# Performance work log

Measured on AMD Instinct MI355X. Metric: run time of the kernel, lower is better.

Reference implementation:

```python
import jax, jax.numpy as jnp
import numpy as np
from jax import lax

STRIDE = 2  # down_sample_stride
MATMUL_NORM = True


def maxpool2d_5d(x, s):
    # x: [B, T, C, H, W]; kernel=s, stride=s, padding=(s-1)//2 == 0 for s=2
    return lax.reduce_window(
        x, -jnp.inf, lax.max,
        window_dimensions=(1, 1, 1, s, s),
        window_strides=(1, 1, 1, s, s),
        padding='VALID')


def setup_inputs() -> dict:
    key = jax.random.key(0)
    k1, k2, k3, k4 = jax.random.split(key, 4)
    B, T, Ck, Cv, H, W = 2, 4, 64, 256, 64, 64
    return {
        'memory_keys': jax.random.normal(k1, (B, T, Ck, H, W), jnp.float32),
        'memory_values': jax.random.normal(k2, (B, T, Cv, H, W), jnp.float32),
        'query_key': jax.random.normal(k3, (B, Ck, H, W), jnp.float32),
        'query_value': jax.random.normal(k4, (B, Cv, H, W), jnp.float32),
    }


def reference(memory_keys, memory_values, query_key, query_value):
    B, T, Ck, oH, oW = memory_keys.shape
    Cv = memory_values.shape[2]
    # down-sample memory bank (max pool, stride 2, no padding)
    mk = maxpool2d_5d(memory_keys, STRIDE)   # [B,T,Ck,h,w]
    mv = maxpool2d_5d(memory_values, STRIDE) # [B,T,Cv,h,w]
    h, w = mk.shape[-2], mk.shape[-1]
    M = T * h * w
    N = oH * oH  # code uses ori_height*ori_height (square assumed)
    # permute(0,2,1,3,4).view(B,Ck,M).permute(0,2,1) -> [B, M, Ck]
    mk = mk.transpose(0, 2, 1, 3, 4).reshape(B, Ck, M).transpose(0, 2, 1)
    qk = query_key.reshape(B, Ck, N)
    attn = jnp.einsum('bmc,bcn->bmn', mk, qk)  # [B, M, N]
    if MATMUL_NORM:
        attn = attn * (Ck ** -0.5)
    attn = jax.nn.softmax(attn, axis=1)  # softmax over memory positions
    mv = mv.transpose(0, 2, 1, 3, 4).reshape(B, Cv, M)
    memory = jnp.einsum('bcm,bmn->bcn', mv, attn).reshape(B, Cv, oH, oW)
    return jnp.concatenate([query_value, memory], axis=1)  # [B, 2*Cv, H, W]
```

## Files before the change

### kernel.cpp

```cpp
#include <hip/hip_runtime.h>
#include <hip/hip_bf16.h>

typedef unsigned short u16;
typedef unsigned int   u32;
typedef __attribute__((ext_vector_type(8))) short  bf16x8;
typedef __attribute__((ext_vector_type(4))) float  floatx4;

#define NB 2
#define NT 4
#define CK 64
#define CV 256
#define HH 64
#define WW 64
#define MM 4096
#define NN 4096
#define SCALE 0.125f
#define SHIFT 4.0f
#define OUT_B 2097152
#define NW 32
#define NIT 32

__device__ __forceinline__ u16 f2b(float f) {
    __hip_bfloat16 h = __float2bfloat16(f);
    union { __hip_bfloat16 h; u16 u; } v; v.h = h; return v.u;
}

#define PRE_K 65536
#define PRE_V 589824
#define PRE_T 1114112

__global__ void prep(const float* __restrict__ mk, const float* __restrict__ mv,
                     const float4* __restrict__ qv,
                     u16* __restrict__ pk2, u16* __restrict__ vt,
                     float* __restrict__ out) {
    int u = blockIdx.x * 256 + threadIdx.x;
    if (u < PRE_K) {
        int m = u & 4095, cb8 = (u >> 12) & 7, b = u >> 15;
        int t = m >> 10, hh = (m >> 5) & 31, ww = m & 31;
        const float* s0 = mk + ((size_t)((b*NT + t)*CK + cb8*8))*(HH*WW)
                             + (2*hh)*WW + 2*ww;
        bf16x8 fr;
        #pragma unroll
        for (int i = 0; i < 8; ++i) {
            const float* s = s0 + (size_t)i*(HH*WW);
            float2 r0 = *(const float2*)s;
            float2 r1 = *(const float2*)(s + WW);
            fr[i] = (short)f2b(fmaxf(fmaxf(r0.x, r0.y), fmaxf(r1.x, r1.y)));
        }
        *(bf16x8*)(pk2 + ((size_t)(b*8 + cb8)*MM + m)*8) = fr;
    } else if (u < PRE_V) {
        int u2 = u - PRE_K;
        int m4 = u2 & 1023, c = (u2 >> 10) & 255, b = u2 >> 18;
        int t = m4 >> 8, hh = (m4 >> 3) & 31, w8 = m4 & 7;
        const float* s0 = mv + ((size_t)((b*NT + t)*CV + c))*(HH*WW)
                             + (2*hh)*WW + 8*w8;
        float4 a0 = *(const float4*)(s0);
        float4 a1 = *(const float4*)(s0 + 4);
        float4 b0 = *(const float4*)(s0 + WW);
        float4 b1 = *(const float4*)(s0 + WW + 4);
        ushort4 r;
        r.x = f2b(fmaxf(fmaxf(a0.x, a0.y), fmaxf(b0.x, b0.y)));
        r.y = f2b(fmaxf(fmaxf(a0.z, a0.w), fmaxf(b0.z, b0.w)));
        r.z = f2b(fmaxf(fmaxf(a1.x, a1.y), fmaxf(b1.x, b1.y)));
        r.w = f2b(fmaxf(fmaxf(a1.z, a1.w), fmaxf(b1.z, b1.w)));
        *(ushort4*)(vt + ((size_t)(b*CV + c)*MM) + m4*4) = r;
    } else {
        int u3 = u - PRE_V;
        int b = u3 >> 18, ru = u3 & 262143;
        ((float4*)out)[(size_t)b*(OUT_B/4) + ru] = qv[u3];
    }
}

__device__ __forceinline__ void qk_phase(bf16x8 k0, bf16x8 k1,
        const bf16x8 (&qf)[2][2], float (&sacc)[2],
        u16* __restrict__ Pd, int lrow, int cbw, int sw)
{
    #pragma unroll
    for (int t = 0; t < 2; ++t) {
        floatx4 s = __builtin_amdgcn_mfma_f32_16x16x32_bf16(
                        k0, qf[0][t], (floatx4){0.f,0.f,0.f,0.f}, 0, 0, 0);
        s = __builtin_amdgcn_mfma_f32_16x16x32_bf16(k1, qf[1][t], s, 0, 0, 0);
        float p0 = __expf(s[0]*SCALE - SHIFT);
        float p1 = __expf(s[1]*SCALE - SHIFT);
        float p2 = __expf(s[2]*SCALE - SHIFT);
        float p3 = __expf(s[3]*SCALE - SHIFT);
        sacc[t] += (p0 + p1) + (p2 + p3);
        u32 d0 = (u32)f2b(p0) | ((u32)f2b(p1) << 16);
        u32 d1 = (u32)f2b(p2) | ((u32)f2b(p3) << 16);
        *(uint2*)&Pd[(t*16 + lrow)*128 + ((cbw ^ sw) << 2)] = make_uint2(d0, d1);
    }
}

__device__ __forceinline__ void pv_phase(const bf16x8 (&vf)[4][2],
        floatx4 (&oacc)[2][2], const u16* __restrict__ Ps,
        int lrow, int quad, int sw)
{
    #pragma unroll
    for (int cc = 0; cc < 4; ++cc) {
        bf16x8 pf[2];
        #pragma unroll
        for (int t = 0; t < 2; ++t) {
            int cb = (cc << 3) + (quad << 1);
            pf[t] = *(const bf16x8*)&Ps[(t*16 + lrow)*128 + ((cb ^ sw) << 2)];
        }
        __builtin_amdgcn_s_setprio(1);
        #pragma unroll
        for (int j = 0; j < 2; ++j)
            #pragma unroll
            for (int t = 0; t < 2; ++t)
                oacc[j][t] = __builtin_amdgcn_mfma_f32_16x16x32_bf16(
                                 vf[cc][j], pf[t], oacc[j][t], 0, 0, 0);
        __builtin_amdgcn_s_setprio(0);
    }
}

__launch_bounds__(512, 2)
__global__ void attn_v2(const u16* __restrict__ pk2, const u16* __restrict__ vt,
                        const float* __restrict__ qk, float* __restrict__ out) {
    const int bid = blockIdx.x;
    const int xcd = bid & 7;
    const int b   = xcd >> 2;
    const int ntile = ((bid >> 3) << 2) + (xcd & 3);
    const int tid = threadIdx.x, w = tid >> 6, l = tid & 63;
    const int lrow = l & 15, quad = l >> 4;
    const int n0 = ntile * NW;
    const int sw = lrow << 1;
    const int cbw = (w << 2) + quad;

    __shared__ u16  P[2][NW * 128];
    __shared__ float sums_s[8][NW];

    bf16x8 qf[2][2];
    const float* qb = qk + (size_t)b * CK * NN + n0;
    #pragma unroll
    for (int cc = 0; cc < 2; ++cc)
        #pragma unroll
        for (int t = 0; t < 2; ++t)
            #pragma unroll
            for (int i = 0; i < 8; ++i) {
                int c = cc*32 + quad*8 + i;
                qf[cc][t][i] = (short)f2b(qb[(size_t)c*NN + t*16 + lrow]);
            }

    const u16* pkb  = pk2 + (size_t)b * (8*MM*8);
    const u16* vtb  = vt  + (size_t)b * CV * MM;
    const int  mrw  = w*16 + lrow;
    const u16* vrow = vtb + (size_t)(w*32 + lrow)*MM + quad*8;

    floatx4 oacc[2][2];
    #pragma unroll
    for (int j = 0; j < 2; ++j)
        #pragma unroll
        for (int t = 0; t < 2; ++t)
            oacc[j][t] = (floatx4){0.f, 0.f, 0.f, 0.f};
    float sacc[2] = {0.f, 0.f};

    bf16x8 vf[4][2];
    {
        bf16x8 k0 = *(const bf16x8*)(pkb + ((size_t)quad*MM + mrw)*8);
        bf16x8 k1 = *(const bf16x8*)(pkb + ((size_t)(quad+4)*MM + mrw)*8);
        #pragma unroll
        for (int cc = 0; cc < 4; ++cc)
            #pragma unroll
            for (int j = 0; j < 2; ++j)
                vf[cc][j] = *(const bf16x8*)(vrow + (size_t)j*(16*MM) + cc*32);
        qk_phase(k0, k1, qf, sacc, P[0], lrow, cbw, sw);
    }

    #pragma unroll 2
    for (int it = 0; it < NIT; ++it) {
        __syncthreads();
        const bool more = (it + 1 < NIT);
        bf16x8 k0n, k1n, vfn[4][2];
        if (more) {
            const int mb2 = (it + 1) << 7;
            k0n = *(const bf16x8*)(pkb + ((size_t)quad*MM + mb2 + mrw)*8);
            k1n = *(const bf16x8*)(pkb + ((size_t)(quad+4)*MM + mb2 + mrw)*8);
            #pragma unroll
            for (int cc = 0; cc < 4; ++cc)
                #pragma unroll
                for (int j = 0; j < 2; ++j)
                    vfn[cc][j] = *(const bf16x8*)(vrow + (size_t)j*(16*MM) + mb2 + cc*32);
        }
        pv_phase(vf, oacc, P[it & 1], lrow, quad, sw);
        if (more) {
            qk_phase(k0n, k1n, qf, sacc, P[(it + 1) & 1], lrow, cbw, sw);
            #pragma unroll
            for (int cc = 0; cc < 4; ++cc)
                #pragma unroll
                for (int j = 0; j < 2; ++j)
                    vf[cc][j] = vfn[cc][j];
        }
    }

    #pragma unroll
    for (int t = 0; t < 2; ++t) {
        float v = sacc[t];
        v += __shfl_xor(v, 16, 64);
        v += __shfl_xor(v, 32, 64);
        if (l < 16) sums_s[w][t*16 + l] = v;
    }
    __syncthreads();
    float inv[2];
    #pragma unroll
    for (int t = 0; t < 2; ++t) {
        float d = 0.f;
        #pragma unroll
        for (int w2 = 0; w2 < 8; ++w2) d += sums_s[w2][t*16 + lrow];
        inv[t] = 1.0f / d;
    }

    float* ob = out + ((size_t)(b*512 + 256))*NN + n0;
    #pragma unroll
    for (int j = 0; j < 2; ++j)
        #pragma unroll
        for (int t = 0; t < 2; ++t)
            #pragma unroll
            for (int r = 0; r < 4; ++r) {
                int c = w*32 + j*16 + quad*4 + r;
                ob[(size_t)c*NN + t*16 + lrow] = oacc[j][t][r] * inv[t];
            }
}


__global__ void pool_v_f32(const float* __restrict__ src, float* __restrict__ out) {
    int e = blockIdx.x * 256 + threadIdx.x;
    int c = e & 255;
    int r = e >> 8;
    int ww = r & 31;  int hh = (r >> 5) & 31;
    int t  = (r >> 10) & 3;  int b = r >> 12;
    int m  = r & (MM - 1);
    const float* s = src + ((size_t)(((b*NT + t)*CV + c)*HH + 2*hh))*WW + 2*ww;
    out[(size_t)b*OUT_B + (size_t)m*CV + c] = fmaxf(fmaxf(s[0], s[1]), fmaxf(s[WW], s[WW+1]));
}

__global__ void pool_k_f32(const float* __restrict__ src, float* __restrict__ dst) {
    int e = blockIdx.x * 256 + threadIdx.x;
    int c = e & 63;
    int r = e >> 6;
    int ww = r & 31;  int hh = (r >> 5) & 31;
    int t  = (r >> 10) & 3;  int b = r >> 12;
    const float* s = src + ((size_t)(((b*NT + t)*CK + c)*HH + 2*hh))*WW + 2*ww;
    dst[e] = fmaxf(fmaxf(s[0], s[1]), fmaxf(s[WW], s[WW+1]));
}

__global__ void copy_qv_f32(const float4* __restrict__ src, float4* __restrict__ dst) {
    int u = blockIdx.x * 256 + threadIdx.x;
    int b  = u >> 18;
    int ru = u & 262143;
    dst[(size_t)b * (OUT_B/4) + ru] = src[u];
}

template<bool STAGED_K>
__launch_bounds__(256)
__global__ void attn_old(const float* __restrict__ pk,
                         const float* __restrict__ mk,
                         const float* __restrict__ qk,
                         float* __restrict__ out) {
    __shared__ __align__(16) float q_lds[CK][4];
    __shared__ __align__(16) float sarr[4][MM];
    __shared__ float inv_l[4];

    const int tid = threadIdx.x;
    const int blk = blockIdx.x;
    const int b   = blk >> 10;
    const int n0  = (blk & 1023) << 2;

    {
        int c = tid >> 2, qi = tid & 3;
        q_lds[c][qi] = qk[((size_t)(b*CK + c))*NN + n0 + qi];
    }
    __syncthreads();

    #pragma unroll
    for (int i = 0; i < 16; ++i) {
        int m = tid + (i << 8);
        float a0 = 0.f, a1 = 0.f, a2 = 0.f, a3 = 0.f;
        if (STAGED_K) {
            const float4* k4 = reinterpret_cast<const float4*>(pk + ((size_t)b*MM + m)*CK);
            #pragma unroll
            for (int cc = 0; cc < 16; ++cc) {
                float4 kv = k4[cc];
                int c = cc*4;
                float4 q0 = *reinterpret_cast<const float4*>(&q_lds[c][0]);
                float4 q1 = *reinterpret_cast<const float4*>(&q_lds[c+1][0]);
                float4 q2 = *reinterpret_cast<const float4*>(&q_lds[c+2][0]);
                float4 q3 = *reinterpret_cast<const float4*>(&q_lds[c+3][0]);
                a0 += kv.x*q0.x + kv.y*q1.x + kv.z*q2.x + kv.w*q3.x;
                a1 += kv.x*q0.y + kv.y*q1.y + kv.z*q2.y + kv.w*q3.y;
                a2 += kv.x*q0.z + kv.y*q1.z + kv.z*q2.z + kv.w*q3.z;
                a3 += kv.x*q0.w + kv.y*q1.w + kv.z*q2.w + kv.w*q3.w;
            }
        } else {
            int ww = m & 31, hh = (m >> 5) & 31, t = m >> 10;
            const float* base = mk + ((size_t)((b*NT + t)*CK)*HH + 2*hh)*WW + 2*ww;
            for (int c = 0; c < CK; ++c) {
                const float* s = base + (size_t)c*HH*WW;
                float kv = fmaxf(fmaxf(s[0], s[1]), fmaxf(s[WW], s[WW+1]));
                float4 q = *reinterpret_cast<const float4*>(&q_lds[c][0]);
                a0 += kv*q.x; a1 += kv*q.y; a2 += kv*q.z; a3 += kv*q.w;
            }
        }
        sarr[0][m] = a0*SCALE;
        sarr[1][m] = a1*SCALE;
        sarr[2][m] = a2*SCALE;
        sarr[3][m] = a3*SCALE;
    }
    __syncthreads();

    const int wave = tid >> 6, lane = tid & 63;
    float mx = -3.0e38f;
    for (int m = lane; m < MM; m += 64) mx = fmaxf(mx, sarr[wave][m]);
    #pragma unroll
    for (int off = 32; off > 0; off >>= 1) mx = fmaxf(mx, __shfl_xor(mx, off, 64));
    float ls = 0.f;
    for (int m = lane; m < MM; m += 64) {
        float p = __expf(sarr[wave][m] - mx);
        sarr[wave][m] = p;
        ls += p;
    }
    #pragma unroll
    for (int off = 32; off > 0; off >>= 1) ls += __shfl_xor(ls, off, 64);
    if (lane == 0) inv_l[wave] = 1.0f / ls;
    __syncthreads();

    const int c4 = lane;
    const float4* vb = reinterpret_cast<const float4*>(out + (size_t)b*OUT_B) + c4;
    const float* prow = sarr[wave];
    float a0 = 0.f, a1 = 0.f, a2 = 0.f, a3 = 0.f;
    for (int m = 0; m < MM; m += 4) {
        float4 p4 = *reinterpret_cast<const float4*>(prow + m);
        const float4* vp = vb + (size_t)m*(CV/4);
        float4 v0 = vp[0], v1 = vp[CV/4], v2 = vp[CV/2], v3 = vp[3*(CV/4)];
        a0 += p4.x*v0.x + p4.y*v1.x + p4.z*v2.x + p4.w*v3.x;
        a1 += p4.x*v0.y + p4.y*v1.y + p4.z*v2.y + p4.w*v3.y;
        a2 += p4.x*v0.z + p4.y*v1.z + p4.z*v2.z + p4.w*v3.z;
        a3 += p4.x*v0.w + p4.y*v1.w + p4.z*v2.w + p4.w*v3.w;
    }

    float inv = inv_l[wave];
    int n = n0 + wave;
    size_t ob = ((size_t)(b*512 + 256 + c4*4))*NN + n;
    out[ob]        = a0*inv;
    out[ob + NN]   = a1*inv;
    out[ob + 2*NN] = a2*inv;
    out[ob + 3*NN] = a3*inv;
}


extern "C" void kernel_launch(void* const* d_in, const int* in_sizes, int n_in,
                              void* d_out, int out_size, void* d_ws, size_t ws_size,
                              hipStream_t stream) {
    const float* mk = (const float*)d_in[0];
    const float* mv = (const float*)d_in[1];
    const float* qk = (const float*)d_in[2];
    const float* qv = (const float*)d_in[3];
    float* out = (float*)d_out;

    u16* pk2 = (u16*)d_ws;
    u16* vt  = pk2 + (size_t)NB*8*MM*8;
    const size_t need = ((size_t)NB*8*MM*8 + (size_t)NB*CV*MM) * sizeof(u16);

    if (ws_size >= need) {
        prep<<<PRE_T/256, 256, 0, stream>>>(mk, mv, (const float4*)qv, pk2, vt, out);
        attn_v2<<<256, 512, 0, stream>>>(pk2, vt, qk, out);
    } else {
        const size_t pk_bytes = (size_t)NB*MM*CK*sizeof(float);
        const bool staged = (ws_size >= pk_bytes);
        float* pk = (float*)d_ws;
        pool_v_f32<<<(NB*MM*CV)/256, 256, 0, stream>>>(mv, out);
        if (staged) {
            pool_k_f32<<<(NB*MM*CK)/256, 256, 0, stream>>>(mk, pk);
            attn_old<true ><<<NB*(NN/4), 256, 0, stream>>>(pk, mk, qk, out);
        } else {
            attn_old<false><<<NB*(NN/4), 256, 0, stream>>>(pk, mk, qk, out);
        }
        copy_qv_f32<<<((NB*CV*HH*WW)/4)/256, 256, 0, stream>>>((const float4*)qv, (float4*)out);
    }
}
```

Measured before the change: 161.0 us.

## Widen attention query tile and split value channels across block pairs

The attention kernel now handles 64 query columns per block instead of 32, and splits the 256 value channels into two halves handled by separate blocks chosen from the XCD index. Each block streams half as much of the value matrix per query column, which cuts V traffic and register pressure for V fragments. The price is that QK scores and their exponentials are computed twice, once per channel half, so QK MFMA and exp work doubles. The main loop is also restructured to peel the final PV step instead of branching on a 'more' flag.

```diff
diff --git a/kernel.cpp b/kernel.cpp
--- a/kernel.cpp
+++ b/kernel.cpp
@@ -17,7 +17,7 @@
 #define SCALE 0.125f
 #define SHIFT 4.0f
 #define OUT_B 2097152
-#define NW 32
+#define NW 64
 #define NIT 32
 
 __device__ __forceinline__ u16 f2b(float f) {
@@ -72,11 +72,11 @@
 }
 
 __device__ __forceinline__ void qk_phase(bf16x8 k0, bf16x8 k1,
-        const bf16x8 (&qf)[2][2], float (&sacc)[2],
+        const bf16x8 (&qf)[2][4], float (&sacc)[4],
         u16* __restrict__ Pd, int lrow, int cbw, int sw)
 {
     #pragma unroll
-    for (int t = 0; t < 2; ++t) {
+    for (int t = 0; t < 4; ++t) {
         floatx4 s = __builtin_amdgcn_mfma_f32_16x16x32_bf16(
                         k0, qf[0][t], (floatx4){0.f,0.f,0.f,0.f}, 0, 0, 0);
         s = __builtin_amdgcn_mfma_f32_16x16x32_bf16(k1, qf[1][t], s, 0, 0, 0);
@@ -91,51 +91,49 @@
     }
 }
 
-__device__ __forceinline__ void pv_phase(const bf16x8 (&vf)[4][2],
-        floatx4 (&oacc)[2][2], const u16* __restrict__ Ps,
+__device__ __forceinline__ void pv_phase(const bf16x8 (&vf)[4],
+        floatx4 (&oacc)[4], const u16* __restrict__ Ps,
         int lrow, int quad, int sw)
 {
     #pragma unroll
     for (int cc = 0; cc < 4; ++cc) {
-        bf16x8 pf[2];
-        #pragma unroll
-        for (int t = 0; t < 2; ++t) {
+        bf16x8 pf[4];
+        #pragma unroll
+        for (int t = 0; t < 4; ++t) {
             int cb = (cc << 3) + (quad << 1);
             pf[t] = *(const bf16x8*)&Ps[(t*16 + lrow)*128 + ((cb ^ sw) << 2)];
         }
         __builtin_amdgcn_s_setprio(1);
         #pragma unroll
-        for (int j = 0; j < 2; ++j)
-            #pragma unroll
-            for (int t = 0; t < 2; ++t)
-                oacc[j][t] = __builtin_amdgcn_mfma_f32_16x16x32_bf16(
-                                 vf[cc][j], pf[t], oacc[j][t], 0, 0, 0);
+        for (int t = 0; t < 4; ++t)
+            oacc[t] = __builtin_amdgcn_mfma_f32_16x16x32_bf16(
+                          vf[cc], pf[t], oacc[t], 0, 0, 0);
         __builtin_amdgcn_s_setprio(0);
     }
 }
 
 __launch_bounds__(512, 2)
-__global__ void attn_v2(const u16* __restrict__ pk2, const u16* __restrict__ vt,
+__global__ void attn_v3(const u16* __restrict__ pk2, const u16* __restrict__ vt,
                         const float* __restrict__ qk, float* __restrict__ out) {
     const int bid = blockIdx.x;
-    const int xcd = bid & 7;
-    const int b   = xcd >> 2;
-    const int ntile = ((bid >> 3) << 2) + (xcd & 3);
+    const int xcd = bid & 7, grp = bid >> 3;
+    const int b   = xcd >> 2, cs = (xcd >> 1) & 1;
+    const int ntile = (xcd & 1) * 32 + grp;
     const int tid = threadIdx.x, w = tid >> 6, l = tid & 63;
     const int lrow = l & 15, quad = l >> 4;
     const int n0 = ntile * NW;
-    const int sw = lrow << 1;
+    const int sw  = lrow << 1;
     const int cbw = (w << 2) + quad;
 
     __shared__ u16  P[2][NW * 128];
     __shared__ float sums_s[8][NW];
 
-    bf16x8 qf[2][2];
+    bf16x8 qf[2][4];
     const float* qb = qk + (size_t)b * CK * NN + n0;
     #pragma unroll
     for (int cc = 0; cc < 2; ++cc)
         #pragma unroll
-        for (int t = 0; t < 2; ++t)
+        for (int t = 0; t < 4; ++t)
             #pragma unroll
             for (int i = 0; i < 8; ++i) {
                 int c = cc*32 + quad*8 + i;
@@ -143,83 +141,64 @@
             }
 
     const u16* pkb  = pk2 + (size_t)b * (8*MM*8);
-    const u16* vtb  = vt  + (size_t)b * CV * MM;
     const int  mrw  = w*16 + lrow;
-    const u16* vrow = vtb + (size_t)(w*32 + lrow)*MM + quad*8;
-
-    floatx4 oacc[2][2];
-    #pragma unroll
-    for (int j = 0; j < 2; ++j)
-        #pragma unroll
-        for (int t = 0; t < 2; ++t)
-            oacc[j][t] = (floatx4){0.f, 0.f, 0.f, 0.f};
-    float sacc[2] = {0.f, 0.f};
-
-    bf16x8 vf[4][2];
-    {
-        bf16x8 k0 = *(const bf16x8*)(pkb + ((size_t)quad*MM + mrw)*8);
-        bf16x8 k1 = *(const bf16x8*)(pkb + ((size_t)(quad+4)*MM + mrw)*8);
+    const u16* vrow = vt + ((size_t)b*CV + cs*128 + w*16 + lrow)*MM + quad*8;
+
+    floatx4 oacc[4];
+    #pragma unroll
+    for (int t = 0; t < 4; ++t) oacc[t] = (floatx4){0.f, 0.f, 0.f, 0.f};
+    float sacc[4] = {0.f, 0.f, 0.f, 0.f};
+
+    bf16x8 k0 = *(const bf16x8*)(pkb + ((size_t)quad*MM + mrw)*8);
+    bf16x8 k1 = *(const bf16x8*)(pkb + ((size_t)(quad+4)*MM + mrw)*8);
+    bf16x8 vf[4];
+    #pragma unroll
+    for (int cc = 0; cc < 4; ++cc)
+        vf[cc] = *(const bf16x8*)(vrow + cc*32);
+    qk_phase(k0, k1, qf, sacc, P[0], lrow, cbw, sw);
+
+    for (int it = 0; it < NIT - 1; ++it) {
+        __syncthreads();
+        const int mb2 = (it + 1) << 7;
+        bf16x8 k0n = *(const bf16x8*)(pkb + ((size_t)quad*MM + mb2 + mrw)*8);
+        bf16x8 k1n = *(const bf16x8*)(pkb + ((size_t)(quad+4)*MM + mb2 + mrw)*8);
+        bf16x8 vn[4];
         #pragma unroll
         for (int cc = 0; cc < 4; ++cc)
-            #pragma unroll
-            for (int j = 0; j < 2; ++j)
-                vf[cc][j] = *(const bf16x8*)(vrow + (size_t)j*(16*MM) + cc*32);
-        qk_phase(k0, k1, qf, sacc, P[0], lrow, cbw, sw);
-    }
-
-    #pragma unroll 2
-    for (int it = 0; it < NIT; ++it) {
-        __syncthreads();
-        const bool more = (it + 1 < NIT);
-        bf16x8 k0n, k1n, vfn[4][2];
-        if (more) {
-            const int mb2 = (it + 1) << 7;
-            k0n = *(const bf16x8*)(pkb + ((size_t)quad*MM + mb2 + mrw)*8);
-            k1n = *(const bf16x8*)(pkb + ((size_t)(quad+4)*MM + mb2 + mrw)*8);
-            #pragma unroll
-            for (int cc = 0; cc < 4; ++cc)
-                #pragma unroll
-                for (int j = 0; j < 2; ++j)
-                    vfn[cc][j] = *(const bf16x8*)(vrow + (size_t)j*(16*MM) + mb2 + cc*32);
-        }
+            vn[cc] = *(const bf16x8*)(vrow + mb2 + cc*32);
         pv_phase(vf, oacc, P[it & 1], lrow, quad, sw);
-        if (more) {
-            qk_phase(k0n, k1n, qf, sacc, P[(it + 1) & 1], lrow, cbw, sw);
-            #pragma unroll
-            for (int cc = 0; cc < 4; ++cc)
-                #pragma unroll
-                for (int j = 0; j < 2; ++j)
-                    vf[cc][j] = vfn[cc][j];
-        }
-    }
-
-    #pragma unroll
-    for (int t = 0; t < 2; ++t) {
+        qk_phase(k0n, k1n, qf, sacc, P[(it + 1) & 1], lrow, cbw, sw);
+        #pragma unroll
+        for (int cc = 0; cc < 4; ++cc) vf[cc] = vn[cc];
+    }
+    __syncthreads();
+    pv_phase(vf, oacc, P[(NIT - 1) & 1], lrow, quad, sw);
+
+    #pragma unroll
+    for (int t = 0; t < 4; ++t) {
         float v = sacc[t];
         v += __shfl_xor(v, 16, 64);
         v += __shfl_xor(v, 32, 64);
         if (l < 16) sums_s[w][t*16 + l] = v;
     }
     __syncthreads();
-    float inv[2];
-    #pragma unroll
-    for (int t = 0; t < 2; ++t) {
+    float inv[4];
+    #pragma unroll
+    for (int t = 0; t < 4; ++t) {
         float d = 0.f;
         #pragma unroll
         for (int w2 = 0; w2 < 8; ++w2) d += sums_s[w2][t*16 + lrow];
         inv[t] = 1.0f / d;
     }
 
-    float* ob = out + ((size_t)(b*512 + 256))*NN + n0;
-    #pragma unroll
-    for (int j = 0; j < 2; ++j)
-        #pragma unroll
-        for (int t = 0; t < 2; ++t)
-            #pragma unroll
-            for (int r = 0; r < 4; ++r) {
-                int c = w*32 + j*16 + quad*4 + r;
-                ob[(size_t)c*NN + t*16 + lrow] = oacc[j][t][r] * inv[t];
-            }
+    float* ob = out + ((size_t)(b*512 + 256 + cs*128))*NN + n0;
+    #pragma unroll
+    for (int t = 0; t < 4; ++t)
+        #pragma unroll
+        for (int r = 0; r < 4; ++r) {
+            int c_loc = w*16 + quad*4 + r;
+            ob[(size_t)c_loc*NN + t*16 + lrow] = oacc[t][r] * inv[t];
+        }
 }
 
 
@@ -363,7 +342,7 @@
 
     if (ws_size >= need) {
         prep<<<PRE_T/256, 256, 0, stream>>>(mk, mv, (const float4*)qv, pk2, vt, out);
-        attn_v2<<<256, 512, 0, stream>>>(pk2, vt, qk, out);
+        attn_v3<<<256, 512, 0, stream>>>(pk2, vt, qk, out);
     } else {
         const size_t pk_bytes = (size_t)NB*MM*CK*sizeof(float);
         const bool staged = (ws_size >= pk_bytes);
```

Result: faster. 143.7 us (-10.7%).
